# Kernel tuning notes

Measured on AMD Instinct MI355X. Metric: run time of the kernel, lower is better.

## Reference

```python
import jax, jax.numpy as jnp
import numpy as np

B, T, C = 4, 2048, 2048
N_HEAD = 16
HEAD_DIM = C // N_HEAD


def rotate_half(x):
    # interleaved rotate: pairs (x0,x1),(x2,x3),... -> (-x1,x0),(-x3,x2),...
    x1 = x[..., ::2]
    x2 = x[..., 1::2]
    return jnp.stack((-x2, x1), axis=-1).reshape(x.shape)


def compute_rope(seq_len, head_dim, dtype):
    inv_freq = 1.0 / (10000.0 ** (jnp.arange(0, head_dim, 2, dtype=jnp.float32) / head_dim))
    t = jnp.arange(seq_len, dtype=jnp.float32)
    freqs = t[:, None] * inv_freq[None, :]            # [T, head_dim/2]
    emb = jnp.concatenate((freqs, freqs), axis=-1)    # [T, head_dim] (module cats freqs twice)
    cos = jnp.cos(emb)[None, None, :, :].astype(dtype)
    sin = jnp.sin(emb)[None, None, :, :].astype(dtype)
    return cos, sin


def setup_inputs() -> dict:
    key = jax.random.key(0)
    k1, k2, k3, k4, k5 = jax.random.split(key, 5)
    s = 1.0 / np.sqrt(C)
    return {
        "x": jax.random.normal(k1, (B, T, C), dtype=jnp.float32),
        "Wqkv": jax.random.normal(k2, (C, 3 * C), dtype=jnp.float32) * s,
        "bqkv": jnp.zeros((3 * C,), dtype=jnp.float32),
        "Wproj": jax.random.normal(k3, (C, C), dtype=jnp.float32) * s,
        "bproj": jnp.zeros((C,), dtype=jnp.float32),
    }


def reference(x, Wqkv, bqkv, Wproj, bproj):
    Bx, Tx, Cx = x.shape
    qkv = x @ Wqkv + bqkv                              # [B,T,3C]
    q, k, v = jnp.split(qkv, 3, axis=2)
    # -> [B, H, T, D]
    q = q.reshape(Bx, Tx, N_HEAD, HEAD_DIM).transpose(0, 2, 1, 3)
    k = k.reshape(Bx, Tx, N_HEAD, HEAD_DIM).transpose(0, 2, 1, 3)
    v = v.reshape(Bx, Tx, N_HEAD, HEAD_DIM).transpose(0, 2, 1, 3)
    cos, sin = compute_rope(Tx, HEAD_DIM, x.dtype)
    q = q * cos + rotate_half(q) * sin
    k = k * cos + rotate_half(k) * sin
    scale = 1.0 / jnp.sqrt(jnp.asarray(HEAD_DIM, x.dtype))
    scores = jnp.einsum('bhqd,bhkd->bhqk', q, k) * scale
    causal = jnp.tril(jnp.ones((Tx, Tx), dtype=bool))
    scores = jnp.where(causal[None, None, :, :], scores, jnp.asarray(-jnp.inf, x.dtype))
    attn = jax.nn.softmax(scores, axis=-1)
    y = jnp.einsum('bhqk,bhkd->bhqd', attn, v)          # [B,H,T,D]
    y = y.transpose(0, 2, 1, 3).reshape(Bx, Tx, Cx)
    return y @ Wproj + bproj
```

## Files before the change

### kernel.cpp

```cpp
#include <hip/hip_runtime.h>
#include <hip/hip_bf16.h>
#include <stdint.h>

#define DEV __device__ __forceinline__
#define WAITV(n) asm volatile("s_waitcnt vmcnt(" #n ")" ::: "memory")
#define WAITLGKM0 asm volatile("s_waitcnt lgkmcnt(0)" ::: "memory")
#define SCHEDB __builtin_amdgcn_sched_barrier(0)

typedef __attribute__((ext_vector_type(4))) float f32x4;
typedef __attribute__((ext_vector_type(8))) short bf16x8;
typedef unsigned short u16;

constexpr int Bb = 4, Tt = 2048, Ccn = 2048, NHn = 16, HDn = 128;
constexpr int MM = Bb * Tt;
constexpr int NQKV = 3 * Ccn;
constexpr int KD = 2048;
constexpr size_t K2 = (size_t)KD * 2;
constexpr float QSCALE = 0.08838834764831845f;

DEV u16 f2bf(float f) {
  __hip_bfloat16 h = __float2bfloat16(f);
  return *reinterpret_cast<u16*>(&h);
}

DEV void gl_lds16(const void* g, void* l) {
  __builtin_amdgcn_global_load_lds(
      (const __attribute__((address_space(1))) void*)g,
      (__attribute__((address_space(3))) void*)l, 16, 0, 0);
}


__global__ void k_rope_table(float* __restrict__ ct, float* __restrict__ st) {
  int idx = blockIdx.x * blockDim.x + threadIdx.x;
  if (idx >= Tt * 64) return;
  int t = idx >> 6, j = idx & 63;
  float invf = expf(-(float)j * 0.14391157f);
  float a = (float)t * invf;
  ct[idx] = cosf(a);
  st[idx] = sinf(a);
}

__global__ void k_cvt(const float* __restrict__ in, u16* __restrict__ out, int n) {
  int i = blockIdx.x * blockDim.x + threadIdx.x;
  int stride = gridDim.x * blockDim.x;
  int n4 = n >> 2;
  for (int idx = i; idx < n4; idx += stride) {
    float4 v = ((const float4*)in)[idx];
    ushort4 o;
    o.x = f2bf(v.x); o.y = f2bf(v.y); o.z = f2bf(v.z); o.w = f2bf(v.w);
    ((ushort4*)out)[idx] = o;
  }
}

__global__ void k_transpose_cvt(const float* __restrict__ in, u16* __restrict__ out,
                                int R, int NC) {
  __shared__ u16 tile[64][72];
  int tr = blockIdx.y * 64, tc = blockIdx.x * 64;
  int r = threadIdx.x >> 2, c = (threadIdx.x & 3) * 16;
  const float* src = in + (size_t)(tr + r) * NC + tc + c;
#pragma unroll
  for (int i = 0; i < 16; i++) tile[r][c + i] = f2bf(src[i]);
  __syncthreads();
  u16* dst = out + (size_t)(tc + r) * R + tr + c;
#pragma unroll
  for (int i = 0; i < 16; i++) dst[i] = tile[c + i][r];
}

__global__ void k_vtrans(const u16* __restrict__ v, u16* __restrict__ vt) {
  __shared__ u16 tile[64][72];
  int bh = blockIdx.z;
  int t0 = blockIdx.x * 64, d0 = blockIdx.y * 64;
  int r = threadIdx.x >> 2, c = (threadIdx.x & 3) * 16;
  const u16* src = v + ((size_t)bh * Tt + t0) * HDn + d0;
#pragma unroll
  for (int i = 0; i < 16; i++) tile[r][c + i] = src[(size_t)r * HDn + c + i];
  __syncthreads();
  u16* dst = vt + ((size_t)bh * HDn + d0) * Tt + t0;
#pragma unroll
  for (int i = 0; i < 16; i++) dst[(size_t)r * Tt + c + i] = tile[c + i][r];
}


template <int MODE>
__global__ __launch_bounds__(512, 2) void k_gemm256(
    const u16* __restrict__ A, const u16* __restrict__ Bt,
    int Ndim, int NBX,
    const float* __restrict__ bias,
    u16* __restrict__ q_r, u16* __restrict__ k_r, u16* __restrict__ v_r,
    const float* __restrict__ ctab, const float* __restrict__ stab,
    float* __restrict__ outp) {
  __shared__ __align__(16) u16 SM[65536];
  const int tid = threadIdx.x;
  const int w = tid >> 6, lane = tid & 63;
  const int l16 = lane & 15, l4 = lane >> 4;
  const int wr = w >> 2, wc = w & 3;
  const int bid = blockIdx.x, nwg = gridDim.x;
  const int swz = (bid & 7) * (nwg >> 3) + (bid >> 3);
  const int by = swz / NBX, bx = swz % NBX;
  const int m0 = by * 256, n0 = bx * 256;
  constexpr int NT = KD >> 6;
  constexpr int NIT = NT >> 1;

  const int Mx = (l16 & 7) << 4;
  const int b6 = Mx & 64;
  const int lane_lo = l16 * 128 + ((l4 * 16) ^ (Mx & 48));
  const char* const pA0 = (const char*)SM + wr * 16384 + lane_lo + b6;
  const char* const pA1 = (const char*)SM + wr * 16384 + lane_lo + (64 - b6);
  const char* const pB0 = (const char*)SM + 65536 + (wc >> 1) * 16384 + (wc & 1) * 8192 + lane_lo + b6;
  const char* const pB1 = (const char*)SM + 65536 + (wc >> 1) * 16384 + (wc & 1) * 8192 + lane_lo + (64 - b6);

  size_t soff[2];
#pragma unroll
  for (int i = 0; i < 2; i++) {
    int op = i * 8192 + tid * 16;
    int ol = op ^ (((op >> 7) & 7) << 4);
    int row = ol >> 7, colb = ol & 127;
    soff[i] = (size_t)row * K2 + (size_t)colb;
  }
  const char* srcA[2][2];
  const char* srcB[2][2];
#pragma unroll
  for (int hh = 0; hh < 2; hh++)
#pragma unroll
    for (int i = 0; i < 2; i++) {
      srcA[hh][i] = (const char*)A + (size_t)(m0 + hh * 128) * K2 + soff[i];
      srcB[hh][i] = (const char*)Bt + (size_t)(n0 + hh * 128) * K2 + soff[i];
    }
  char* const dstBase = (char*)SM;

  auto stA = [&](int buf, int half, int kt) {
#pragma unroll
    for (int i = 0; i < 2; i++)
      gl_lds16(srcA[half][i] + (size_t)kt * 128,
               dstBase + buf * 32768 + half * 16384 + i * 8192 + tid * 16);
  };
  auto stB = [&](int buf, int half, int kt) {
#pragma unroll
    for (int i = 0; i < 2; i++)
      gl_lds16(srcB[half][i] + (size_t)kt * 128,
               dstBase + 65536 + buf * 32768 + half * 16384 + i * 8192 + tid * 16);
  };

  f32x4 acc[8][4];
  const f32x4 zf = {0.f, 0.f, 0.f, 0.f};
#pragma unroll
  for (int i = 0; i < 8; i++)
#pragma unroll
    for (int j = 0; j < 4; j++) acc[i][j] = zf;

  stA(0, 0, 0); stA(0, 1, 0); stB(0, 0, 0); stB(0, 1, 0);
  stB(1, 0, 1); stB(1, 1, 1);
  WAITV(4);
  __builtin_amdgcn_s_barrier();

  bf16x8 bfrag[4][2];
  for (int I = 0; I < NIT; ++I) {
    const int t1 = 2 * I + 1, t2 = 2 * I + 2, t3 = 2 * I + 3;
#pragma unroll
    for (int buf = 0; buf < 2; ++buf) {
#pragma unroll
      for (int ph = 0; ph < 4; ++ph) {
        const int gp = buf * 4 + ph;
        if (ph == 0) {
#pragma unroll
          for (int nj = 0; nj < 4; nj++) {
            bfrag[nj][0] = *(const bf16x8*)(pB0 + buf * 32768 + nj * 2048);
            bfrag[nj][1] = *(const bf16x8*)(pB1 + buf * 32768 + nj * 2048);
          }
        }
        bf16x8 af[2][2];
#pragma unroll
        for (int dm = 0; dm < 2; dm++) {
          af[dm][0] = *(const bf16x8*)(pA0 + buf * 32768 + (ph * 2 + dm) * 2048);
          af[dm][1] = *(const bf16x8*)(pA1 + buf * 32768 + (ph * 2 + dm) * 2048);
        }
        SCHEDB;
        if (gp == 0)      stA(1, 0, t1);
        else if (gp == 1) stA(1, 1, t1);
        else if (gp == 2) { if (t2 < NT) stB(0, 0, t2); }
        else if (gp == 3) {
          if (t2 < NT) stB(0, 1, t2);
          if (I < NIT - 1) { WAITV(4); } else { WAITV(0); }
        }
        else if (gp == 4) { if (t2 < NT) stA(0, 0, t2); }
        else if (gp == 5) { if (t2 < NT) stA(0, 1, t2); }
        else if (gp == 6) { if (t3 < NT) stB(1, 0, t3); }
        else if (gp == 7) { if (t3 < NT) { stB(1, 1, t3); WAITV(4); } }
        __builtin_amdgcn_s_barrier();
        WAITLGKM0;
        SCHEDB;
        __builtin_amdgcn_s_setprio(1);
#pragma unroll
        for (int ks = 0; ks < 2; ks++)
#pragma unroll
          for (int dm = 0; dm < 2; dm++)
#pragma unroll
            for (int nj = 0; nj < 4; nj++)
              acc[ph * 2 + dm][nj] = __builtin_amdgcn_mfma_f32_16x16x32_bf16(
                  af[dm][ks], bfrag[nj][ks], acc[ph * 2 + dm][nj], 0, 0, 0);
        __builtin_amdgcn_s_setprio(0);
        __builtin_amdgcn_s_barrier();
      }
    }
  }

  if constexpr (MODE == 1) {
#pragma unroll
    for (int mi = 0; mi < 8; mi++) {
      const int mrow = m0 + wr * 128 + mi * 16 + l4 * 4;
#pragma unroll
      for (int nj = 0; nj < 4; nj++) {
        const int col = n0 + wc * 64 + nj * 16 + l16;
        const float bi = bias[col];
#pragma unroll
        for (int jj = 0; jj < 4; jj++)
          outp[(size_t)(mrow + jj) * Ndim + col] = acc[mi][nj][jj] + bi;
      }
    }
  } else {
#pragma unroll
    for (int mi = 0; mi < 8; mi++) {
      const int mrow = m0 + wr * 128 + mi * 16 + l4 * 4;
#pragma unroll
      for (int nj = 0; nj < 4; nj++) {
        const int n = n0 + wc * 64 + nj * 16 + l16;
        const float bi = bias[n];
        const int part = n >> 11;
        const int hcol = n & 2047;
        const int h = hcol >> 7, d = hcol & 127;
        const int dm = d & 63;
#pragma unroll
        for (int jj = 0; jj < 4; jj++) {
          const int m = mrow + jj;
          const int b = m >> 11, t = m & 2047;
          float val = acc[mi][nj][jj] + bi;
          size_t didx = (((size_t)b * NHn + h) * Tt + t) * HDn + d;
          if (part == 2) {
            v_r[didx] = f2bf(val);
          } else {
            float partner = __shfl_xor(val, 1);
            float rh = (d & 1) ? partner : -partner;
            float cs = ctab[t * 64 + dm], sn = stab[t * 64 + dm];
            float o = val * cs + rh * sn;
            if (part == 0) q_r[didx] = f2bf(o * QSCALE);
            else           k_r[didx] = f2bf(o);
          }
        }
      }
    }
  }
}

__global__ __launch_bounds__(256, 2) void k_attn(
    const u16* __restrict__ q_r, const u16* __restrict__ k_r,
    const u16* __restrict__ vt, u16* __restrict__ y) {
  __shared__ u16 Ks[2][64 * 128];
  __shared__ u16 Vs[128 * 64];
  __shared__ u16 Ps[4][32 * 72];
  const int lin = blockIdx.x;
  const int swz = (lin & 7) * 64 + (lin >> 3);
  const int qpair = swz & 7;
  const int bh = swz >> 3;
  const int tid = threadIdx.x, w = tid >> 6, lane = tid & 63;
  const int l16 = lane & 15, l4 = lane >> 4;
  const int b = bh >> 4, h = bh & 15;

  const u16* kbase = k_r + (size_t)bh * Tt * HDn;
  const u16* vbase = vt + (size_t)bh * HDn * Tt;
  const f32x4 zf = {0.f, 0.f, 0.f, 0.f};

  auto stageK = [&](int buf, int j) {
    const char* ksrc = (const char*)(kbase + (size_t)j * 64 * HDn);
#pragma unroll
    for (int i = 0; i < 4; i++) {
      int op = tid * 16 + i * 4096;
      int ol = op ^ (((op >> 8) & 7) << 4);
      gl_lds16(ksrc + ol, (char*)&Ks[buf][0] + op);
    }
  };
  auto stageV = [&](int j) {
    const char* vsrc = (const char*)(vbase + (size_t)j * 64);
#pragma unroll
    for (int i = 0; i < 4; i++) {
      int op = tid * 16 + i * 4096;
      int ol = op ^ (((op >> 7) & 7) << 4);
      int row = ol >> 7, colb = ol & 127;
      gl_lds16(vsrc + (size_t)row * (Tt * 2) + colb, (char*)Vs + op);
    }
  };

#pragma unroll
  for (int qsel = 0; qsel < 2; ++qsel) {
    const int qt = qsel ? (15 - qpair) : qpair;

    const u16* qbase = q_r + ((size_t)bh * Tt + qt * 128 + w * 32) * HDn;
    bf16x8 qf[2][4];
#pragma unroll
    for (int mi = 0; mi < 2; mi++)
#pragma unroll
      for (int kc = 0; kc < 4; kc++)
        qf[mi][kc] = *(const bf16x8*)(qbase + (size_t)(mi * 16 + l16) * HDn + kc * 32 + l4 * 8);

    f32x4 acc_o[2][8];
#pragma unroll
    for (int mi = 0; mi < 2; mi++)
#pragma unroll
      for (int nf = 0; nf < 8; nf++) acc_o[mi][nf] = zf;
    float mrow[2][4], lrow[2][4];
#pragma unroll
    for (int mi = 0; mi < 2; mi++)
#pragma unroll
      for (int jj = 0; jj < 4; jj++) { mrow[mi][jj] = -1e30f; lrow[mi][jj] = 0.f; }

    const int ntiles = 2 * qt + 2;
    stageK(0, 0);
    __syncthreads();
    int cur = 0;

    for (int j = 0; j < ntiles; ++j) {
      const bool more = (j + 1 < ntiles);
      stageV(j);
      if (more) stageK(cur ^ 1, j + 1);

      f32x4 s[2][4];
#pragma unroll
      for (int mi = 0; mi < 2; mi++)
#pragma unroll
        for (int nj = 0; nj < 4; nj++) s[mi][nj] = zf;
#pragma unroll
      for (int kc = 0; kc < 4; kc++) {
        bf16x8 kf[4];
#pragma unroll
        for (int nj = 0; nj < 4; nj++) {
          int row = nj * 16 + l16;
          kf[nj] = *(const bf16x8*)((const char*)&Ks[cur][0] + row * 256 +
                                    ((kc * 64 + l4 * 16) ^ ((row & 7) << 4)));
        }
        __builtin_amdgcn_s_setprio(1);
#pragma unroll
        for (int mi = 0; mi < 2; mi++)
#pragma unroll
          for (int nj = 0; nj < 4; nj++)
            s[mi][nj] = __builtin_amdgcn_mfma_f32_16x16x32_bf16(qf[mi][kc], kf[nj], s[mi][nj], 0, 0, 0);
        __builtin_amdgcn_s_setprio(0);
      }

      const bool diag = (j >= 2 * qt);
#pragma unroll
      for (int mi = 0; mi < 2; mi++) {
#pragma unroll
        for (int jj = 0; jj < 4; jj++) {
          if (diag) {
            const int qrow = qt * 128 + w * 32 + mi * 16 + l4 * 4 + jj;
#pragma unroll
            for (int nj = 0; nj < 4; nj++) {
              const int key = j * 64 + nj * 16 + l16;
              if (key > qrow) s[mi][nj][jj] = -1e30f;
            }
          }
          float lm = fmaxf(fmaxf(s[mi][0][jj], s[mi][1][jj]), fmaxf(s[mi][2][jj], s[mi][3][jj]));
#pragma unroll
          for (int dd = 1; dd < 16; dd <<= 1) lm = fmaxf(lm, __shfl_xor(lm, dd));
          if (lm > mrow[mi][jj]) {
            const float sc = __expf(mrow[mi][jj] - lm);
            mrow[mi][jj] = lm;
            lrow[mi][jj] *= sc;
#pragma unroll
            for (int nf = 0; nf < 8; nf++) acc_o[mi][nf][jj] *= sc;
          }
          float ps = 0.f;
#pragma unroll
          for (int nj = 0; nj < 4; nj++) {
            float p = __expf(s[mi][nj][jj] - mrow[mi][jj]);
            s[mi][nj][jj] = p;
            ps += p;
          }
#pragma unroll
          for (int dd = 1; dd < 16; dd <<= 1) ps += __shfl_xor(ps, dd);
          lrow[mi][jj] += ps;
          const int prow = mi * 16 + l4 * 4 + jj;
#pragma unroll
          for (int nj = 0; nj < 4; nj++)
            Ps[w][prow * 72 + nj * 16 + l16] = f2bf(s[mi][nj][jj]);
        }
      }

      if (more) { WAITV(4); } else { WAITV(0); }
      __builtin_amdgcn_s_barrier();

#pragma unroll
      for (int kc = 0; kc < 2; kc++) {
        bf16x8 pf[2];
#pragma unroll
        for (int mi = 0; mi < 2; mi++)
          pf[mi] = *(const bf16x8*)((const char*)&Ps[w][0] + (mi * 16 + l16) * 144 + kc * 64 + l4 * 16);
        bf16x8 vf[8];
#pragma unroll
        for (int nf = 0; nf < 8; nf++) {
          int row = nf * 16 + l16;
          vf[nf] = *(const bf16x8*)((const char*)Vs + row * 128 +
                                    ((kc * 64 + l4 * 16) ^ ((row & 7) << 4)));
        }
        __builtin_amdgcn_s_setprio(1);
#pragma unroll
        for (int nf = 0; nf < 8; nf++)
#pragma unroll
          for (int mi = 0; mi < 2; mi++)
            acc_o[mi][nf] = __builtin_amdgcn_mfma_f32_16x16x32_bf16(pf[mi], vf[nf], acc_o[mi][nf], 0, 0, 0);
        __builtin_amdgcn_s_setprio(0);
      }
      __syncthreads();
      cur ^= 1;
    }

#pragma unroll
    for (int mi = 0; mi < 2; mi++) {
#pragma unroll
      for (int jj = 0; jj < 4; jj++) {
        const float rinv = 1.f / lrow[mi][jj];
        const int t = qt * 128 + w * 32 + mi * 16 + l4 * 4 + jj;
        u16* yrow = y + ((size_t)b * Tt + t) * Ccn + h * HDn;
#pragma unroll
        for (int nf = 0; nf < 8; nf++)
          yrow[nf * 16 + l16] = f2bf(acc_o[mi][nf][jj] * rinv);
      }
    }
    __syncthreads();
  }
}


extern "C" void kernel_launch(void* const* d_in, const int* in_sizes, int n_in,
                              void* d_out, int out_size, void* d_ws, size_t ws_size,
                              hipStream_t stream) {
  const float* x     = (const float*)d_in[0];
  const float* Wqkv  = (const float*)d_in[1];
  const float* bqkv  = (const float*)d_in[2];
  const float* Wproj = (const float*)d_in[3];
  const float* bproj = (const float*)d_in[4];
  float* out = (float*)d_out;
  char* ws = (char*)d_ws;

  size_t off = 0;
  auto alloc = [&](size_t bytes) -> char* {
    char* p = ws + off;
    off += (bytes + 255) & ~(size_t)255;
    return p;
  };
  float* ctab  = (float*)alloc((size_t)Tt * 64 * sizeof(float));
  float* stab  = (float*)alloc((size_t)Tt * 64 * sizeof(float));
  u16* xb      = (u16*)alloc((size_t)MM * Ccn * 2);
  u16* WqkvT   = (u16*)alloc((size_t)NQKV * Ccn * 2);
  u16* WprojT  = (u16*)alloc((size_t)Ccn * Ccn * 2);
  u16* q_rb    = (u16*)alloc((size_t)MM * Ccn * 2);
  u16* k_rb    = (u16*)alloc((size_t)MM * Ccn * 2);
  u16* v_rb    = (u16*)alloc((size_t)MM * Ccn * 2);
  u16* ybuf    = (u16*)alloc((size_t)MM * Ccn * 2);
  u16* vtb     = xb;

  k_rope_table<<<(Tt * 64 + 255) / 256, 256, 0, stream>>>(ctab, stab);
  k_cvt<<<1024, 256, 0, stream>>>(x, xb, MM * Ccn);
  k_transpose_cvt<<<dim3(NQKV / 64, Ccn / 64), 256, 0, stream>>>(Wqkv, WqkvT, Ccn, NQKV);
  k_transpose_cvt<<<dim3(Ccn / 64, Ccn / 64), 256, 0, stream>>>(Wproj, WprojT, Ccn, Ccn);

  k_gemm256<0><<<dim3((MM / 256) * (NQKV / 256)), 512, 0, stream>>>(
      xb, WqkvT, NQKV, NQKV / 256, bqkv, q_rb, k_rb, v_rb, ctab, stab, nullptr);

  k_vtrans<<<dim3(Tt / 64, HDn / 64, Bb * NHn), 256, 0, stream>>>(v_rb, vtb);

  k_attn<<<dim3(512), 256, 0, stream>>>(q_rb, k_rb, vtb, ybuf);

  k_gemm256<1><<<dim3((MM / 256) * (Ccn / 256)), 512, 0, stream>>>(
      ybuf, WprojT, Ccn, Ccn / 256, bproj, nullptr, nullptr, nullptr, nullptr, nullptr, out);
}
```

Measured before the change: 516.6 us.

## Software-pipeline LDS fragment reads one phase ahead of MFMA in GEMM loop

Restructures the GEMM main loop so the A and B fragments for the next phase are read from LDS into double-buffered registers while the current phase's MFMAs run, using partial lgkmcnt waits instead of a full wait. It also drops one of the two barriers per phase and peels the last iteration so no bounds checks are needed. The aim is to hide LDS read latency and cut barrier overhead. In exchange it uses more registers, which may lower occupancy, and the looser barriers and waits raise race risk if the counts are wrong.

```diff
diff --git a/kernel.cpp b/kernel.cpp
--- a/kernel.cpp
+++ b/kernel.cpp
@@ -4,7 +4,7 @@
 
 #define DEV __device__ __forceinline__
 #define WAITV(n) asm volatile("s_waitcnt vmcnt(" #n ")" ::: "memory")
-#define WAITLGKM0 asm volatile("s_waitcnt lgkmcnt(0)" ::: "memory")
+#define WAITL(n) asm volatile("s_waitcnt lgkmcnt(" #n ")" ::: "memory")
 #define SCHEDB __builtin_amdgcn_sched_barrier(0)
 
 typedef __attribute__((ext_vector_type(4))) float f32x4;
@@ -141,66 +141,90 @@
                dstBase + 65536 + buf * 32768 + half * 16384 + i * 8192 + tid * 16);
   };
 
+  bf16x8 af[2][2][2];
+  bf16x8 bfr[2][4][2];
   f32x4 acc[8][4];
   const f32x4 zf = {0.f, 0.f, 0.f, 0.f};
 #pragma unroll
   for (int i = 0; i < 8; i++)
 #pragma unroll
     for (int j = 0; j < 4; j++) acc[i][j] = zf;
+
+  auto rdAfrag = [&](int par, int bufsel, int ph) {
+#pragma unroll
+    for (int dm = 0; dm < 2; dm++) {
+      af[par][dm][0] = *(const bf16x8*)(pA0 + bufsel * 32768 + (ph * 2 + dm) * 2048);
+      af[par][dm][1] = *(const bf16x8*)(pA1 + bufsel * 32768 + (ph * 2 + dm) * 2048);
+    }
+  };
+  auto rdBfrag = [&](int bufsel) {
+#pragma unroll
+    for (int nj = 0; nj < 4; nj++) {
+      bfr[bufsel][nj][0] = *(const bf16x8*)(pB0 + bufsel * 32768 + nj * 2048);
+      bfr[bufsel][nj][1] = *(const bf16x8*)(pB1 + bufsel * 32768 + nj * 2048);
+    }
+  };
+  auto mfma16 = [&](int par, int bufsel, int ph) {
+    __builtin_amdgcn_s_setprio(1);
+#pragma unroll
+    for (int ks = 0; ks < 2; ks++)
+#pragma unroll
+      for (int dm = 0; dm < 2; dm++)
+#pragma unroll
+        for (int nj = 0; nj < 4; nj++)
+          acc[ph * 2 + dm][nj] = __builtin_amdgcn_mfma_f32_16x16x32_bf16(
+              af[par][dm][ks], bfr[bufsel][nj][ks], acc[ph * 2 + dm][nj], 0, 0, 0);
+    __builtin_amdgcn_s_setprio(0);
+  };
 
   stA(0, 0, 0); stA(0, 1, 0); stB(0, 0, 0); stB(0, 1, 0);
   stB(1, 0, 1); stB(1, 1, 1);
   WAITV(4);
   __builtin_amdgcn_s_barrier();
-
-  bf16x8 bfrag[4][2];
-  for (int I = 0; I < NIT; ++I) {
+  SCHEDB;
+  rdBfrag(0);
+  rdAfrag(0, 0, 0);
+
+  for (int I = 0; I < NIT - 1; ++I) {
     const int t1 = 2 * I + 1, t2 = 2 * I + 2, t3 = 2 * I + 3;
 #pragma unroll
-    for (int buf = 0; buf < 2; ++buf) {
-#pragma unroll
-      for (int ph = 0; ph < 4; ++ph) {
-        const int gp = buf * 4 + ph;
-        if (ph == 0) {
-#pragma unroll
-          for (int nj = 0; nj < 4; nj++) {
-            bfrag[nj][0] = *(const bf16x8*)(pB0 + buf * 32768 + nj * 2048);
-            bfrag[nj][1] = *(const bf16x8*)(pB1 + buf * 32768 + nj * 2048);
-          }
-        }
-        bf16x8 af[2][2];
-#pragma unroll
-        for (int dm = 0; dm < 2; dm++) {
-          af[dm][0] = *(const bf16x8*)(pA0 + buf * 32768 + (ph * 2 + dm) * 2048);
-          af[dm][1] = *(const bf16x8*)(pA1 + buf * 32768 + (ph * 2 + dm) * 2048);
-        }
-        SCHEDB;
-        if (gp == 0)      stA(1, 0, t1);
-        else if (gp == 1) stA(1, 1, t1);
-        else if (gp == 2) { if (t2 < NT) stB(0, 0, t2); }
-        else if (gp == 3) {
-          if (t2 < NT) stB(0, 1, t2);
-          if (I < NIT - 1) { WAITV(4); } else { WAITV(0); }
-        }
-        else if (gp == 4) { if (t2 < NT) stA(0, 0, t2); }
-        else if (gp == 5) { if (t2 < NT) stA(0, 1, t2); }
-        else if (gp == 6) { if (t3 < NT) stB(1, 0, t3); }
-        else if (gp == 7) { if (t3 < NT) { stB(1, 1, t3); WAITV(4); } }
-        __builtin_amdgcn_s_barrier();
-        WAITLGKM0;
-        SCHEDB;
-        __builtin_amdgcn_s_setprio(1);
-#pragma unroll
-        for (int ks = 0; ks < 2; ks++)
-#pragma unroll
-          for (int dm = 0; dm < 2; dm++)
-#pragma unroll
-            for (int nj = 0; nj < 4; nj++)
-              acc[ph * 2 + dm][nj] = __builtin_amdgcn_mfma_f32_16x16x32_bf16(
-                  af[dm][ks], bfrag[nj][ks], acc[ph * 2 + dm][nj], 0, 0, 0);
-        __builtin_amdgcn_s_setprio(0);
-        __builtin_amdgcn_s_barrier();
-      }
+    for (int gp = 0; gp < 8; ++gp) {
+      __builtin_amdgcn_s_barrier();
+      SCHEDB;
+      if (gp < 3)        rdAfrag((gp + 1) & 1, 0, gp + 1);
+      else if (gp == 3)  { rdBfrag(1); rdAfrag(0, 1, 0); }
+      else if (gp < 7)   rdAfrag((gp + 1) & 1, 1, gp - 3);
+      else               { rdBfrag(0); rdAfrag(0, 0, 0); }
+      if (gp == 0)       stA(1, 0, t1);
+      else if (gp == 1)  stA(1, 1, t1);
+      else if (gp == 2)  { stB(0, 0, t2); WAITV(2); }
+      else if (gp == 3)  stB(0, 1, t2);
+      else if (gp == 4)  stA(0, 0, t2);
+      else if (gp == 5)  stA(0, 1, t2);
+      else if (gp == 6)  { stB(1, 0, t3); WAITV(2); }
+      else               stB(1, 1, t3);
+      if (gp == 3 || gp == 7) { WAITL(12); } else { WAITL(4); }
+      SCHEDB;
+      mfma16(gp & 1, gp >> 2, gp & 3);
+    }
+  }
+  {
+    const int t1 = 2 * (NIT - 1) + 1;
+#pragma unroll
+    for (int gp = 0; gp < 8; ++gp) {
+      __builtin_amdgcn_s_barrier();
+      SCHEDB;
+      if (gp < 3)        rdAfrag((gp + 1) & 1, 0, gp + 1);
+      else if (gp == 3)  { rdBfrag(1); rdAfrag(0, 1, 0); }
+      else if (gp < 7)   rdAfrag((gp + 1) & 1, 1, gp - 3);
+      if (gp == 0)       stA(1, 0, t1);
+      else if (gp == 1)  stA(1, 1, t1);
+      else if (gp == 2)  WAITV(0);
+      if (gp == 3)       { WAITL(12); }
+      else if (gp == 7)  { WAITL(0); }
+      else               { WAITL(4); }
+      SCHEDB;
+      mfma16(gp & 1, gp >> 2, gp & 3);
     }
   }
 
```

Result: slower. 562.6 us (+8.9%).
